# Optimization experiments

Measured on AMD Instinct MI355X. Metric: run time of the kernel, lower is better.

## Reference

```python
import jax, jax.numpy as jnp
import numpy as np

S, E, K, D = 50000, 20000, 128, 128  # students, exercises, knowledge, emb dim
NE = 800000                          # edges per polarity
B = 8192                             # batch of response logs
L = 3                                # gcn layers
TEMP, CONTROL = 0.2, 0.3


def setup_inputs() -> dict:
    key = jax.random.key(0)
    ks = jax.random.split(key, 40)

    def nrm(i, shape, scale=0.05):
        return jax.random.normal(ks[i], shape, jnp.float32) * scale

    def uni(i, shape):
        return jax.random.uniform(ks[i], shape, jnp.float32)

    inp = {
        'stu_id': jax.random.randint(ks[0], (B,), 0, S, jnp.int32),
        'exer_id': jax.random.randint(ks[1], (B,), 0, E, jnp.int32),
        'kn_emb': uni(2, (B, K)),
        'ui1_u': jax.random.randint(ks[3], (NE,), 0, S, jnp.int32),
        'ui1_i': jax.random.randint(ks[4], (NE,), 0, E, jnp.int32),
        'ui1_val': uni(5, (NE,)), 'iu1_val': uni(6, (NE,)),
        'eps_ui1': uni(7, (NE,)), 'eps_iu1': uni(8, (NE,)),
        'ui0_u': jax.random.randint(ks[9], (NE,), 0, S, jnp.int32),
        'ui0_i': jax.random.randint(ks[10], (NE,), 0, E, jnp.int32),
        'ui0_val': uni(11, (NE,)), 'iu0_val': uni(12, (NE,)),
        'eps_ui0': uni(13, (NE,)), 'eps_iu0': uni(14, (NE,)),
        # embeddings
        'student_emb': nrm(15, (S, D)), 'exercise_emb': nrm(16, (E, D)),
        'knowledge_emb': nrm(17, (K, D)),
        'stu_b': nrm(18, (S, 1)), 'exer_b': nrm(19, (E, 1)), 'disc': nrm(20, (E, 1)),
        # edge-gate MLPs (polarity 1 and 0)
        'W1_l1': nrm(21, (D, 2 * D)), 'b1_l1': jnp.zeros((D,), jnp.float32),
        'W2_l1': nrm(22, (1, D)), 'b2_l1': jnp.zeros((1,), jnp.float32),
        'W1_l0': nrm(23, (D, 2 * D)), 'b1_l0': jnp.zeros((D,), jnp.float32),
        'W2_l0': nrm(24, (1, D)), 'b2_l0': jnp.zeros((1,), jnp.float32),
        # PosLinear prednet
        'pw1': nrm(25, (256, K)), 'pb1': jnp.zeros((256,), jnp.float32),
        'pw2': nrm(26, (128, 256)), 'pb2': jnp.zeros((128,), jnp.float32),
        'pw3': nrm(27, (1, 128)), 'pb3': jnp.zeros((1,), jnp.float32),
    }
    return inp


def _gate(uids, iids, uemb, iemb, W1, b1, W2, b2, eps):
    # concrete-distribution edge gate; embeddings are detached in original code
    row = jax.lax.stop_gradient(uemb)[uids]          # [NE, D]
    col = jax.lax.stop_gradient(iemb)[iids]          # [NE, D]
    h = jax.nn.relu(jnp.concatenate([row, col], axis=1) @ W1.T + b1)
    logit = (h @ W2.T + b2).reshape(-1)              # [NE]
    eps = jnp.clip(eps, 1e-6, 1.0 - 1e-6)
    g = jnp.log(eps) - jnp.log1p(-eps)               # logistic noise
    return CONTROL * jax.nn.sigmoid((logit + g) / TEMP) + (1.0 - CONTROL)


def _spmm(rows, cols, vals, x, n_rows):
    # out[rows] += vals * x[cols]
    return jax.ops.segment_sum(vals[:, None] * x[cols], rows, num_segments=n_rows)


def _poslin(x, W, b):
    Wp = 2.0 * jax.nn.relu(-W) + W  # == |W|
    return x @ Wp.T + b


def reference(stu_id, exer_id, kn_emb, ui1_u, ui1_i, ui1_val, iu1_val, eps_ui1,
              eps_iu1, ui0_u, ui0_i, ui0_val, iu0_val, eps_ui0, eps_iu0,
              student_emb, exercise_emb, knowledge_emb, stu_b, exer_b, disc,
              W1_l1, b1_l1, W2_l1, b2_l1, W1_l0, b1_l0, W2_l0, b2_l0,
              pw1, pb1, pw2, pb2, pw3, pb3):
    # --- graph_learner: per-edge gates on all 4 sparse matrices ---
    v_ui1 = ui1_val * _gate(ui1_u, ui1_i, student_emb, exercise_emb, W1_l1, b1_l1, W2_l1, b2_l1, eps_ui1)
    v_iu1 = iu1_val * _gate(ui1_u, ui1_i, student_emb, exercise_emb, W1_l1, b1_l1, W2_l1, b2_l1, eps_iu1)
    v_ui0 = ui0_val * _gate(ui0_u, ui0_i, student_emb, exercise_emb, W1_l0, b1_l0, W2_l0, b2_l0, eps_ui0)
    v_iu0 = iu0_val * _gate(ui0_u, ui0_i, student_emb, exercise_emb, W1_l0, b1_l0, W2_l0, b2_l0, eps_iu0)

    # --- graph_representations: L rounds of sparse propagation, mean over layers ---
    stu, exer = student_emb, exercise_emb
    stu_sum, exer_sum = stu, exer
    for _ in range(L):
        u1 = _spmm(ui1_u, ui1_i, v_ui1, exer, S)
        i1 = _spmm(ui1_i, ui1_u, v_iu1, stu, E)
        u0 = _spmm(ui0_u, ui0_i, v_ui0, exer, S)
        i0 = _spmm(ui0_i, ui0_u, v_iu0, stu, E)
        stu, exer = u1 + u0, i1 + i0
        stu_sum = stu_sum + stu
        exer_sum = exer_sum + exer
    stu_final = stu_sum / (L + 1)
    exer_final = exer_sum / (L + 1)

    # --- NCDM-style prediction head with PosLinear MLP ---
    stat = jax.nn.sigmoid(stu_final[stu_id] @ knowledge_emb.T + stu_b[stu_id])   # [B, K]
    diff = jax.nn.sigmoid(exer_final[exer_id] @ knowledge_emb.T + exer_b[exer_id])
    e_d = jax.nn.sigmoid(disc[exer_id])                                          # [B, 1]
    x = e_d * (stat - diff) * kn_emb
    h = jax.nn.sigmoid(_poslin(x, pw1, pb1))
    h = jax.nn.sigmoid(_poslin(h, pw2, pb2))
    out = jax.nn.sigmoid(_poslin(h, pw3, pb3)).reshape(-1)                       # [B]
    return out
```

## Files before the change

### kernel.cpp

```cpp
#include <hip/hip_runtime.h>
#include <hip/hip_bf16.h>
#include <math.h>

#define S_N 50000
#define E_N 20000
#define K_N 128
#define D_N 128
#define NE_N 800000
#define B_N 8192
#define L_N 3
#define GATE_TILES (NE_N / 64)
#define NB_S 782
#define NB_E 313
#define BPAD 464
#define BSLACK 480

typedef __attribute__((ext_vector_type(4))) float floatx4;
typedef __attribute__((ext_vector_type(8))) short short8v;

__device__ __forceinline__ unsigned short f2bf(float x) {
  unsigned int u = __float_as_uint(x);
  u += 0x7FFFu + ((u >> 16) & 1u);
  return (unsigned short)(u >> 16);
}
__device__ __forceinline__ float bf2f(unsigned short u) {
  return __uint_as_float(((unsigned int)u) << 16);
}
__device__ __forceinline__ float sigm(float z) { return 1.0f / (1.0f + __expf(-z)); }

__device__ __forceinline__ unsigned char f2e4m3(float x) {
  unsigned int u = __float_as_uint(x);
  unsigned char s = (unsigned char)((u >> 24) & 0x80);
  int e = (int)((u >> 23) & 0xFF) - 127;
  unsigned int m = u & 0x7FFFFF;
  if (((u >> 23) & 0xFF) == 0) return s;
  if (e >= 9) return s | 0x7E;
  if (e < -10) return s;
  if (e >= -6) {
    unsigned int keep = m >> 20;
    unsigned int rest = m & 0xFFFFF;
    if (rest > 0x80000u || (rest == 0x80000u && (keep & 1))) keep++;
    if (keep == 8) { keep = 0; e++; if (e >= 9) return s | 0x7E; }
    unsigned char b = (unsigned char)(s | ((e + 7) << 3) | keep);
    if ((b & 0x7F) == 0x7F) b = s | 0x7E;
    return b;
  }
  int shift = -6 - e;
  unsigned int full = 0x800000u | m;
  unsigned int q = full >> (20 + shift);
  unsigned int rest = full & ((1u << (20 + shift)) - 1);
  unsigned int half = 1u << (19 + shift);
  if (rest > half || (rest == half && (q & 1))) q++;
  if (q == 8) return s | 0x08;
  return (unsigned char)(s | q);
}
__device__ __forceinline__ unsigned int pk4_fp8(float4 v) {
  return (unsigned int)f2e4m3(v.x) | ((unsigned int)f2e4m3(v.y) << 8) |
         ((unsigned int)f2e4m3(v.z) << 16) | ((unsigned int)f2e4m3(v.w) << 24);
}

__global__ void prep_kernel(const float* __restrict__ W1_l1, const float* __restrict__ W1_l0,
                            const float* __restrict__ pw1, const float* __restrict__ pw2,
                            const float* __restrict__ pw3, const float* __restrict__ ke,
                            unsigned int* __restrict__ w1f8_1, unsigned int* __restrict__ w1f8_0,
                            float* __restrict__ pw1T, float* __restrict__ pw2T,
                            float* __restrict__ pw3a, float* __restrict__ keT) {
  int i = blockIdx.x * blockDim.x + threadIdx.x;
  if (i < 8192) { w1f8_1[i] = pk4_fp8(((const float4*)W1_l1)[i]); return; }
  i -= 8192;
  if (i < 8192) { w1f8_0[i] = pk4_fp8(((const float4*)W1_l0)[i]); return; }
  i -= 8192;
  if (i < 32768) { int d = i >> 8, j = i & 255; pw1T[i] = fabsf(pw1[j * 128 + d]); return; }
  i -= 32768;
  if (i < 32768) { int d = i >> 7, j = i & 127; pw2T[i] = fabsf(pw2[j * 256 + d]); return; }
  i -= 32768;
  if (i < 128) { pw3a[i] = fabsf(pw3[i]); return; }
  i -= 128;
  if (i < 16384) { int d = i >> 7, k = i & 127; keT[i] = ke[k * 128 + d]; return; }
}

__global__ void init_bf_kernel(const float* __restrict__ se, const float* __restrict__ ee,
                               unsigned short* __restrict__ sbf, unsigned short* __restrict__ ebf,
                               unsigned int* __restrict__ sf8, unsigned int* __restrict__ ef8,
                               float* __restrict__ sS, float* __restrict__ eS) {
  int i = blockIdx.x * blockDim.x + threadIdx.x;
  const int nS4 = S_N * 32, nE4 = E_N * 32;
  if (i < nS4) {
    float4 v = ((const float4*)se)[i];
    ((float4*)sS)[i] = v;
    unsigned int lo = (unsigned int)f2bf(v.x) | ((unsigned int)f2bf(v.y) << 16);
    unsigned int hi = (unsigned int)f2bf(v.z) | ((unsigned int)f2bf(v.w) << 16);
    ((uint2*)sbf)[i] = make_uint2(lo, hi);
    sf8[i] = pk4_fp8(v);
    return;
  }
  i -= nS4;
  if (i < nE4) {
    float4 v = ((const float4*)ee)[i];
    ((float4*)eS)[i] = v;
    unsigned int lo = (unsigned int)f2bf(v.x) | ((unsigned int)f2bf(v.y) << 16);
    unsigned int hi = (unsigned int)f2bf(v.z) | ((unsigned int)f2bf(v.w) << 16);
    ((uint2*)ebf)[i] = make_uint2(lo, hi);
    ef8[i] = pk4_fp8(v);
  }
}

__global__ void zero_kernel(int* __restrict__ p, int n) {
  int i = blockIdx.x * blockDim.x + threadIdx.x;
  if (i < n) p[i] = 0;
}

__global__ __launch_bounds__(256)
void histB_kernel(const int* __restrict__ u1, const int* __restrict__ i1,
                  const int* __restrict__ u0, const int* __restrict__ i0,
                  int* __restrict__ gHistS, int* __restrict__ gHistE) {
  __shared__ int hS[NB_S], hE[NB_E];
  int t = threadIdx.x;
  for (int b = t; b < NB_S; b += 256) hS[b] = 0;
  for (int b = t; b < NB_E; b += 256) hE[b] = 0;
  __syncthreads();
  int e0 = blockIdx.x * 2048;
  for (int k = 0; k < 8; ++k) {
    int e = e0 + k * 256 + t;
    if (e < NE_N) {
      atomicAdd(&hS[u1[e] >> 6], 1);
      atomicAdd(&hS[u0[e] >> 6], 1);
      atomicAdd(&hE[i1[e] >> 6], 1);
      atomicAdd(&hE[i0[e] >> 6], 1);
    }
  }
  __syncthreads();
  for (int b = t; b < NB_S; b += 256) if (hS[b]) atomicAdd(&gHistS[b], hS[b]);
  for (int b = t; b < NB_E; b += 256) if (hE[b]) atomicAdd(&gHistE[b], hE[b]);
}

__global__ __launch_bounds__(128)
void scanB_kernel(const int* __restrict__ gHistS, int* __restrict__ baseS,
                  int* __restrict__ gCurS, int* __restrict__ basePS,
                  const int* __restrict__ gHistE, int* __restrict__ baseE,
                  int* __restrict__ gCurE, int* __restrict__ basePE) {
  int w = threadIdx.x >> 6, l = threadIdx.x & 63;
  int n = w ? NB_E : NB_S;
  const int* src = w ? gHistE : gHistS;
  int* bs  = w ? baseE  : baseS;
  int* cur = w ? gCurE  : gCurS;
  int* bsP = w ? basePE : basePS;
  int carry = 0, carryP = 0;
  for (int base = 0; base < n; base += 64) {
    int i = base + l;
    int v = (i < n) ? src[i] : 0;
    int p = (i < n) ? ((v + BPAD + 15) & ~15) : 0;
    int x = v, y = p;
#pragma unroll
    for (int o = 1; o < 64; o <<= 1) {
      int xx = __shfl_up(x, o, 64);
      int yy = __shfl_up(y, o, 64);
      if (l >= o) { x += xx; y += yy; }
    }
    if (i < n) {
      int ex = carry + x - v;
      bs[i] = ex; cur[i] = ex;
      bsP[i] = carryP + y - p;
    }
    carry += __shfl(x, 63, 64);
    carryP += __shfl(y, 63, 64);
  }
  if (l == 0) { bs[n] = carry; bsP[n] = carryP; }
}

__global__ __launch_bounds__(256)
void append_kernel(const int* __restrict__ u1, const int* __restrict__ i1,
                   const int* __restrict__ u0, const int* __restrict__ i0,
                   const float* __restrict__ v_ui1, const float* __restrict__ v_iu1,
                   const float* __restrict__ v_ui0, const float* __restrict__ v_iu0,
                   int* __restrict__ gCurS, int* __restrict__ gCurE,
                   int2* __restrict__ recS, int2* __restrict__ recE) {
  __shared__ int hS[NB_S], hE[NB_E];
  int t = threadIdx.x;
  for (int b = t; b < NB_S; b += 256) hS[b] = 0;
  for (int b = t; b < NB_E; b += 256) hE[b] = 0;
  __syncthreads();
  int e0 = blockIdx.x * 2048;
  for (int k = 0; k < 8; ++k) {
    int e = e0 + k * 256 + t;
    if (e < NE_N) {
      atomicAdd(&hS[u1[e] >> 6], 1);
      atomicAdd(&hS[u0[e] >> 6], 1);
      atomicAdd(&hE[i1[e] >> 6], 1);
      atomicAdd(&hE[i0[e] >> 6], 1);
    }
  }
  __syncthreads();
  for (int b = t; b < NB_S; b += 256) { int c = hS[b]; hS[b] = c ? atomicAdd(&gCurS[b], c) : 0; }
  for (int b = t; b < NB_E; b += 256) { int c = hE[b]; hE[b] = c ? atomicAdd(&gCurE[b], c) : 0; }
  __syncthreads();
  for (int k = 0; k < 8; ++k) {
    int e = e0 + k * 256 + t;
    if (e < NE_N) {
      int a = u1[e], b = i1[e], c = u0[e], d = i0[e];
      int s;
      s = atomicAdd(&hS[a >> 6], 1); recS[s] = make_int2(((a & 63) << 16) | b, __float_as_int(v_ui1[e]));
      s = atomicAdd(&hE[b >> 6], 1); recE[s] = make_int2(((b & 63) << 16) | a, __float_as_int(v_iu1[e]));
      s = atomicAdd(&hS[c >> 6], 1); recS[s] = make_int2(((c & 63) << 16) | d, __float_as_int(v_ui0[e]));
      s = atomicAdd(&hE[d >> 6], 1); recE[s] = make_int2(((d & 63) << 16) | c, __float_as_int(v_iu0[e]));
    }
  }
}

__global__ __launch_bounds__(256)
void sortRow_kernel(const int* __restrict__ baseIn, const int* __restrict__ basePad,
                    const int2* __restrict__ rin_all, int2* __restrict__ rout_all,
                    int* __restrict__ rowPtr, int* __restrict__ rowCnt8, int nRowsTot) {
  __shared__ int cntR[64], offR[64], curR[64];
  int b = blockIdx.x, t = threadIdx.x;
  int bi = baseIn[b], cnt = baseIn[b + 1] - bi;
  int bo = basePad[b];
  int row0 = b * 64;
  const int2* rin = rin_all + bi;
  int2* rout = rout_all + bo;
  if (t < 64) cntR[t] = 0;
  __syncthreads();
  for (int j = t; j < cnt; j += 256) atomicAdd(&cntR[(rin[j].x >> 16) & 63], 1);
  __syncthreads();
  if (t < 64) {
    int p = (cntR[t] + 7) & ~7;
    int x = p;
#pragma unroll
    for (int o = 1; o < 64; o <<= 1) { int y = __shfl_up(x, o, 64); if (t >= o) x += y; }
    int ex = x - p;
    offR[t] = ex; curR[t] = ex;
    if (row0 + t < nRowsTot) {
      rowPtr[row0 + t] = bo + ex;
      rowCnt8[row0 + t] = p >> 3;
    }
  }
  __syncthreads();
  for (int j = t; j < cnt; j += 256) {
    int2 rc = rin[j];
    int r = (rc.x >> 16) & 63;
    int slot = atomicAdd(&curR[r], 1);
    rout[slot] = make_int2(rc.x & 0xFFFF, rc.y);
  }
  __syncthreads();
  if (t < 64) {
    int c = cntR[t], p = (c + 7) & ~7, o = offR[t];
    for (int j = c; j < p; ++j) rout[o + j] = make_int2(0, 0);
  }
}

__global__ __launch_bounds__(512, 2)
void gate_kernel(const int* __restrict__ eu1, const int* __restrict__ ei1,
                 const int* __restrict__ eu0, const int* __restrict__ ei0,
                 const unsigned char* __restrict__ sf8, const unsigned char* __restrict__ ef8,
                 const unsigned char* __restrict__ w1f8_1, const unsigned char* __restrict__ w1f8_0,
                 const float* __restrict__ b1_1, const float* __restrict__ w2_1,
                 const float* __restrict__ b2_1,
                 const float* __restrict__ b1_0, const float* __restrict__ w2_0,
                 const float* __restrict__ b2_0,
                 float* __restrict__ logit1, float* __restrict__ logit0) {
  __shared__ unsigned char Xl[64 * 272];
  __shared__ float plds[8][16];
  const int* eu; const int* ei; const unsigned char* w1f8;
  const float *b1p, *w2p, *b2p; float* lg;
  if (blockIdx.x < 2048) {
    eu = eu1; ei = ei1; w1f8 = w1f8_1; b1p = b1_1; w2p = w2_1; b2p = b2_1; lg = logit1;
  } else {
    eu = eu0; ei = ei0; w1f8 = w1f8_0; b1p = b1_0; w2p = w2_0; b2p = b2_0; lg = logit0;
  }
  int bb = blockIdx.x & 2047;
  int t = threadIdx.x;
  int wv = t >> 6, l = t & 63;
  int sub = l & 15, grp = l >> 4;
  int nh = wv & 1, rg = wv >> 1;

  long bfrag[4][8];
#pragma unroll
  for (int nt = 0; nt < 4; ++nt) {
    int col = nh * 64 + nt * 16 + sub;
#pragma unroll
    for (int ks = 0; ks < 8; ++ks)
      bfrag[nt][ks] = *(const long*)&w1f8[(col << 8) + ks * 32 + grp * 8];
  }
  float b1v[4], w2v[4];
#pragma unroll
  for (int nt = 0; nt < 4; ++nt) {
    int col = nh * 64 + nt * 16 + sub;
    b1v[nt] = b1p[col];
    w2v[nt] = w2p[col];
  }
  float b2s = b2p[0];

  for (int tile = bb; tile < GATE_TILES; tile += 2048) {
    int e0 = tile * 64;
    {
      int el = t >> 3, q = t & 7;
      int eIdx = e0 + el;
      const unsigned char* srcrow = (q < 4)
          ? sf8 + (size_t)eu[eIdx] * 128 + q * 32
          : ef8 + (size_t)ei[eIdx] * 128 + (q - 4) * 32;
      uint4 c0 = ((const uint4*)srcrow)[0];
      uint4 c1 = ((const uint4*)srcrow)[1];
      *(uint4*)&Xl[el * 272 + q * 32] = c0;
      *(uint4*)&Xl[el * 272 + q * 32 + 16] = c1;
    }
    __syncthreads();

    floatx4 zero4 = {0.f, 0.f, 0.f, 0.f};
    floatx4 acc[4] = {zero4, zero4, zero4, zero4};
#pragma unroll
    for (int ks = 0; ks < 8; ++ks) {
      long a = *(const long*)&Xl[(rg * 16 + sub) * 272 + ks * 32 + grp * 8];
#pragma unroll
      for (int nt = 0; nt < 4; ++nt)
        acc[nt] = __builtin_amdgcn_mfma_f32_16x16x32_fp8_fp8(a, bfrag[nt][ks], acc[nt], 0, 0, 0);
    }
    float p0 = 0, p1 = 0, p2 = 0, p3 = 0;
#pragma unroll
    for (int nt = 0; nt < 4; ++nt) {
      float bb2 = b1v[nt], ww = w2v[nt];
      p0 += fmaxf(acc[nt][0] + bb2, 0.0f) * ww;
      p1 += fmaxf(acc[nt][1] + bb2, 0.0f) * ww;
      p2 += fmaxf(acc[nt][2] + bb2, 0.0f) * ww;
      p3 += fmaxf(acc[nt][3] + bb2, 0.0f) * ww;
    }
#pragma unroll
    for (int m = 1; m < 16; m <<= 1) {
      p0 += __shfl_xor(p0, m, 64);
      p1 += __shfl_xor(p1, m, 64);
      p2 += __shfl_xor(p2, m, 64);
      p3 += __shfl_xor(p3, m, 64);
    }
    if (sub < 4) {
      float pv = (sub == 0) ? p0 : (sub == 1) ? p1 : (sub == 2) ? p2 : p3;
      plds[wv][grp * 4 + sub] = pv;
    }
    __syncthreads();
    if (wv == 0)
      lg[e0 + l] = plds[(l >> 4) * 2][l & 15] + plds[(l >> 4) * 2 + 1][l & 15] + b2s;
    __syncthreads();
  }
}

__global__ __launch_bounds__(256)
void gatefin_kernel(const float* __restrict__ logit1, const float* __restrict__ logit0,
                    const float* __restrict__ ui1_val, const float* __restrict__ iu1_val,
                    const float* __restrict__ eps_ui1, const float* __restrict__ eps_iu1,
                    const float* __restrict__ ui0_val, const float* __restrict__ iu0_val,
                    const float* __restrict__ eps_ui0, const float* __restrict__ eps_iu0,
                    float* __restrict__ v_ui1, float* __restrict__ v_iu1,
                    float* __restrict__ v_ui0, float* __restrict__ v_iu0) {
  int e = blockIdx.x * 256 + threadIdx.x;
  if (e >= NE_N) return;
  float lg1 = logit1[e], lg0 = logit0[e];
  float ep, g, s;
  ep = fminf(fmaxf(eps_ui1[e], 1e-6f), 1.0f - 1e-6f);
  g = __logf(ep) - log1pf(-ep);
  s = 1.0f / (1.0f + __expf(-(lg1 + g) * 5.0f));
  v_ui1[e] = ui1_val[e] * (0.3f * s + 0.7f);
  ep = fminf(fmaxf(eps_iu1[e], 1e-6f), 1.0f - 1e-6f);
  g = __logf(ep) - log1pf(-ep);
  s = 1.0f / (1.0f + __expf(-(lg1 + g) * 5.0f));
  v_iu1[e] = iu1_val[e] * (0.3f * s + 0.7f);
  ep = fminf(fmaxf(eps_ui0[e], 1e-6f), 1.0f - 1e-6f);
  g = __logf(ep) - log1pf(-ep);
  s = 1.0f / (1.0f + __expf(-(lg0 + g) * 5.0f));
  v_ui0[e] = ui0_val[e] * (0.3f * s + 0.7f);
  ep = fminf(fmaxf(eps_iu0[e], 1e-6f), 1.0f - 1e-6f);
  g = __logf(ep) - log1pf(-ep);
  s = 1.0f / (1.0f + __expf(-(lg0 + g) * 5.0f));
  v_iu0[e] = iu0_val[e] * (0.3f * s + 0.7f);
}

__global__ __launch_bounds__(256)
void spmm_csr_kernel(const int* __restrict__ rowPtrS, const int* __restrict__ rowCnt8S,
                     const int2* __restrict__ rec2S,
                     const int* __restrict__ rowPtrE, const int* __restrict__ rowCnt8E,
                     const int2* __restrict__ rec2E,
                     const unsigned short* __restrict__ scur, const unsigned short* __restrict__ ecur,
                     unsigned short* __restrict__ snxt, unsigned short* __restrict__ enxt,
                     float* __restrict__ stuS, float* __restrict__ exeS) {
  int gw = (blockIdx.x * 256 + threadIdx.x) >> 6;
  int l = threadIdx.x & 63;
  int g = l >> 3, lane8 = l & 7;
  if (gw >= S_N + E_N) return;
  const int2* rec; const unsigned short* src; unsigned short* dst; float* sum;
  const int* rp; const int* rc8; int r;
  if (gw < S_N) { r = gw;       rp = rowPtrS; rc8 = rowCnt8S; rec = rec2S; src = ecur; dst = snxt; sum = stuS; }
  else          { r = gw - S_N; rp = rowPtrE; rc8 = rowCnt8E; rec = rec2E; src = scur; dst = enxt; sum = exeS; }
  int s0 = rp[r], n8 = rc8[r];
  float acc[16];
#pragma unroll
  for (int i = 0; i < 16; ++i) acc[i] = 0.f;
  for (int k = 0; k < n8; ++k) {
    int2 e = rec[s0 + k * 8 + g];
    float val = __int_as_float(e.y);
    const uint4* rowp = (const uint4*)(src + (size_t)e.x * 128);
    uint4 q0 = rowp[lane8 * 2];
    uint4 q1 = rowp[lane8 * 2 + 1];
#pragma unroll
    for (int i = 0; i < 4; ++i) {
      unsigned int w = ((const unsigned int*)&q0)[i];
      acc[2 * i]     = fmaf(val, bf2f((unsigned short)(w & 0xFFFF)), acc[2 * i]);
      acc[2 * i + 1] = fmaf(val, bf2f((unsigned short)(w >> 16)),    acc[2 * i + 1]);
    }
#pragma unroll
    for (int i = 0; i < 4; ++i) {
      unsigned int w = ((const unsigned int*)&q1)[i];
      acc[8 + 2 * i]     = fmaf(val, bf2f((unsigned short)(w & 0xFFFF)), acc[8 + 2 * i]);
      acc[8 + 2 * i + 1] = fmaf(val, bf2f((unsigned short)(w >> 16)),    acc[8 + 2 * i + 1]);
    }
  }
#pragma unroll
  for (int m = 8; m < 64; m <<= 1) {
#pragma unroll
    for (int i = 0; i < 16; ++i) acc[i] += __shfl_xor(acc[i], m, 64);
  }
  if (g == 0) {
    size_t base = (size_t)r * 128 + lane8 * 16;
    short8v o0, o1;
#pragma unroll
    for (int i = 0; i < 8; ++i) { o0[i] = (short)f2bf(acc[i]); o1[i] = (short)f2bf(acc[8 + i]); }
    *(short8v*)(dst + base) = o0;
    *(short8v*)(dst + base + 8) = o1;
    float4* sp = (float4*)(sum + base);
#pragma unroll
    for (int i = 0; i < 4; ++i) {
      float4 s = sp[i];
      s.x += acc[4 * i]; s.y += acc[4 * i + 1]; s.z += acc[4 * i + 2]; s.w += acc[4 * i + 3];
      sp[i] = s;
    }
  }
}

__global__ __launch_bounds__(256)
void head1_kernel(const int* __restrict__ stu_id, const int* __restrict__ exer_id,
                  const float* __restrict__ kn, const float* __restrict__ stuS,
                  const float* __restrict__ exeS, const float* __restrict__ keT,
                  const float* __restrict__ stub, const float* __restrict__ exeb,
                  const float* __restrict__ disc, float* __restrict__ xbuf) {
  __shared__ float srw[4][128], erw[4][128];
  int wv = threadIdx.x >> 6, l = threadIdx.x & 63;
  int b = blockIdx.x * 4 + wv;
  int sid = stu_id[b], eid = exer_id[b];
  float2 sv = ((const float2*)(stuS + (size_t)sid * 128))[l];
  float2 ev = ((const float2*)(exeS + (size_t)eid * 128))[l];
  srw[wv][2 * l] = sv.x * 0.25f; srw[wv][2 * l + 1] = sv.y * 0.25f;
  erw[wv][2 * l] = ev.x * 0.25f; erw[wv][2 * l + 1] = ev.y * 0.25f;
  __syncthreads();
  float s0 = 0, s1 = 0, d0 = 0, d1 = 0;
  for (int d = 0; d < 128; ++d) {
    float sd = srw[wv][d], ed = erw[wv][d];
    float ka = keT[d * 128 + l], kb = keT[d * 128 + l + 64];
    s0 = fmaf(sd, ka, s0); s1 = fmaf(sd, kb, s1);
    d0 = fmaf(ed, ka, d0); d1 = fmaf(ed, kb, d1);
  }
  float sbv = stub[sid], ebv = exeb[eid];
  float edv = sigm(disc[eid]);
  float st0 = sigm(s0 + sbv), st1 = sigm(s1 + sbv);
  float df0 = sigm(d0 + ebv), df1 = sigm(d1 + ebv);
  xbuf[(size_t)b * 128 + l]      = edv * (st0 - df0) * kn[(size_t)b * 128 + l];
  xbuf[(size_t)b * 128 + l + 64] = edv * (st1 - df1) * kn[(size_t)b * 128 + l + 64];
}

__global__ __launch_bounds__(256)
void head2_kernel(const float* __restrict__ xbuf, const float* __restrict__ pw1T,
                  const float* __restrict__ pb1, const float* __restrict__ pw2T,
                  const float* __restrict__ pb2, const float* __restrict__ pw3a,
                  const float* __restrict__ pb3, float* __restrict__ out) {
  __shared__ float xs[4][128], h1s[4][256], h2s[4][128];
  int wv = threadIdx.x >> 6, l = threadIdx.x & 63;
  int b = blockIdx.x * 4 + wv;
  xs[wv][l] = xbuf[(size_t)b * 128 + l];
  xs[wv][l + 64] = xbuf[(size_t)b * 128 + l + 64];
  __syncthreads();
#pragma unroll
  for (int q = 0; q < 4; ++q) {
    int j = q * 64 + l;
    float acc = 0.f;
    for (int d = 0; d < 128; ++d) acc = fmaf(xs[wv][d], pw1T[d * 256 + j], acc);
    h1s[wv][j] = sigm(acc + pb1[j]);
  }
  __syncthreads();
#pragma unroll
  for (int q = 0; q < 2; ++q) {
    int j = q * 64 + l;
    float acc = 0.f;
    for (int d = 0; d < 256; ++d) acc = fmaf(h1s[wv][d], pw2T[d * 128 + j], acc);
    h2s[wv][j] = sigm(acc + pb2[j]);
  }
  __syncthreads();
  float p = h2s[wv][l] * pw3a[l] + h2s[wv][l + 64] * pw3a[l + 64];
#pragma unroll
  for (int m = 1; m < 64; m <<= 1) p += __shfl_xor(p, m, 64);
  if (l == 0) out[b] = sigm(p + pb3[0]);
}

extern "C" void kernel_launch(void* const* d_in, const int* in_sizes, int n_in,
                              void* d_out, int out_size, void* d_ws, size_t ws_size,
                              hipStream_t stream) {
  const int*   stu_id  = (const int*)  d_in[0];
  const int*   exer_id = (const int*)  d_in[1];
  const float* kn_emb  = (const float*)d_in[2];
  const int*   ui1_u   = (const int*)  d_in[3];
  const int*   ui1_i   = (const int*)  d_in[4];
  const float* ui1_val = (const float*)d_in[5];
  const float* iu1_val = (const float*)d_in[6];
  const float* eps_ui1 = (const float*)d_in[7];
  const float* eps_iu1 = (const float*)d_in[8];
  const int*   ui0_u   = (const int*)  d_in[9];
  const int*   ui0_i   = (const int*)  d_in[10];
  const float* ui0_val = (const float*)d_in[11];
  const float* iu0_val = (const float*)d_in[12];
  const float* eps_ui0 = (const float*)d_in[13];
  const float* eps_iu0 = (const float*)d_in[14];
  const float* stu_emb = (const float*)d_in[15];
  const float* exe_emb = (const float*)d_in[16];
  const float* kno_emb = (const float*)d_in[17];
  const float* stu_b   = (const float*)d_in[18];
  const float* exe_b   = (const float*)d_in[19];
  const float* disc    = (const float*)d_in[20];
  const float* W1_l1   = (const float*)d_in[21];
  const float* b1_l1   = (const float*)d_in[22];
  const float* W2_l1   = (const float*)d_in[23];
  const float* b2_l1   = (const float*)d_in[24];
  const float* W1_l0   = (const float*)d_in[25];
  const float* b1_l0   = (const float*)d_in[26];
  const float* W2_l0   = (const float*)d_in[27];
  const float* b2_l0   = (const float*)d_in[28];
  const float* pw1     = (const float*)d_in[29];
  const float* pb1     = (const float*)d_in[30];
  const float* pw2     = (const float*)d_in[31];
  const float* pb2     = (const float*)d_in[32];
  const float* pw3     = (const float*)d_in[33];
  const float* pb3     = (const float*)d_in[34];
  float* out = (float*)d_out;
  (void)in_sizes; (void)n_in; (void)out_size; (void)ws_size;

  size_t off = 0;
  char* base = (char*)d_ws;
  auto carve = [&](size_t bytes) -> char* {
    char* p = base + off;
    off += (bytes + 255) & ~(size_t)255;
    return p;
  };
  unsigned int* w1f8_1 = (unsigned int*)carve(8192 * 4);
  unsigned int* w1f8_0 = (unsigned int*)carve(8192 * 4);
  float* pw1T = (float*)carve(32768 * 4);
  float* pw2T = (float*)carve(32768 * 4);
  float* pw3a = (float*)carve(128 * 4);
  float* keT  = (float*)carve(16384 * 4);
  float* v_ui1 = (float*)carve((size_t)2 * NE_N * 8 + (size_t)BSLACK * NB_S * 8);
  float* v_iu1 = v_ui1 + NE_N;
  float* v_ui0 = v_iu1 + NE_N;
  float* v_iu0 = v_ui0 + NE_N;
  unsigned short* stuBfA = (unsigned short*)carve((size_t)S_N * 128 * 2);
  unsigned short* stuBfB = (unsigned short*)carve((size_t)S_N * 128 * 2);
  unsigned short* exeBfA = (unsigned short*)carve((size_t)E_N * 128 * 2);
  unsigned short* exeBfB = (unsigned short*)carve((size_t)E_N * 128 * 2);
  unsigned int* sf8 = (unsigned int*)carve((size_t)S_N * 32 * 4);
  unsigned int* ef8 = (unsigned int*)carve((size_t)E_N * 32 * 4);
  float* stuS = (float*)carve((size_t)S_N * 128 * 4);
  float* exeS = (float*)carve((size_t)E_N * 128 * 4);
  float* logit1 = (float*)carve((size_t)NE_N * 4);
  float* logit0 = (float*)carve((size_t)NE_N * 4);
  int* gHistS = (int*)carve((size_t)(NB_S + NB_E) * 4);
  int* gHistE = gHistS + NB_S;
  int* baseSb  = (int*)carve((size_t)(NB_S + 1) * 4);
  int* baseEb  = (int*)carve((size_t)(NB_E + 1) * 4);
  int* basePSb = (int*)carve((size_t)(NB_S + 1) * 4);
  int* basePEb = (int*)carve((size_t)(NB_E + 1) * 4);
  int* gCurS  = (int*)carve((size_t)NB_S * 4);
  int* gCurE  = (int*)carve((size_t)NB_E * 4);
  int2* recS = (int2*)carve((size_t)2 * NE_N * 8 + (size_t)BSLACK * NB_E * 8);
  int2* recE = (int2*)carve((size_t)2 * NE_N * 8);
  int* rowPtrS  = (int*)carve((size_t)S_N * 4);
  int* rowCnt8S = (int*)carve((size_t)S_N * 4);
  int* rowPtrE  = (int*)carve((size_t)E_N * 4);
  int* rowCnt8E = (int*)carve((size_t)E_N * 4);
  float* xbuf = (float*)carve((size_t)B_N * 128 * 4);
  int2* rec2S = (int2*)v_ui1;
  int2* rec2E = recS;

  prep_kernel<<<(98432 + 255) / 256, 256, 0, stream>>>(W1_l1, W1_l0, pw1, pw2, pw3, kno_emb,
                                                       w1f8_1, w1f8_0, pw1T, pw2T, pw3a, keT);
  init_bf_kernel<<<(2240000 + 255) / 256, 256, 0, stream>>>(stu_emb, exe_emb, stuBfA, exeBfA,
                                                            sf8, ef8, stuS, exeS);
  zero_kernel<<<(NB_S + NB_E + 255) / 256, 256, 0, stream>>>(gHistS, NB_S + NB_E);
  histB_kernel<<<(NE_N + 2047) / 2048, 256, 0, stream>>>(ui1_u, ui1_i, ui0_u, ui0_i,
                                                         gHistS, gHistE);
  scanB_kernel<<<1, 128, 0, stream>>>(gHistS, baseSb, gCurS, basePSb,
                                      gHistE, baseEb, gCurE, basePEb);
  gate_kernel<<<4096, 512, 0, stream>>>(ui1_u, ui1_i, ui0_u, ui0_i,
                                        (const unsigned char*)sf8, (const unsigned char*)ef8,
                                        (const unsigned char*)w1f8_1, (const unsigned char*)w1f8_0,
                                        b1_l1, W2_l1, b2_l1, b1_l0, W2_l0, b2_l0,
                                        logit1, logit0);
  gatefin_kernel<<<(NE_N + 255) / 256, 256, 0, stream>>>(logit1, logit0,
                                                         ui1_val, iu1_val, eps_ui1, eps_iu1,
                                                         ui0_val, iu0_val, eps_ui0, eps_iu0,
                                                         v_ui1, v_iu1, v_ui0, v_iu0);
  append_kernel<<<(NE_N + 2047) / 2048, 256, 0, stream>>>(ui1_u, ui1_i, ui0_u, ui0_i,
                                                          v_ui1, v_iu1, v_ui0, v_iu0,
                                                          gCurS, gCurE, recS, recE);
  sortRow_kernel<<<NB_S, 256, 0, stream>>>(baseSb, basePSb, recS, rec2S,
                                           rowPtrS, rowCnt8S, S_N);
  sortRow_kernel<<<NB_E, 256, 0, stream>>>(baseEb, basePEb, recE, rec2E,
                                           rowPtrE, rowCnt8E, E_N);
  const unsigned short* scur = stuBfA; const unsigned short* ecur = exeBfA;
  unsigned short* snxt = stuBfB; unsigned short* enxt = exeBfB;
  for (int layer = 0; layer < L_N; ++layer) {
    spmm_csr_kernel<<<(S_N + E_N + 3) / 4, 256, 0, stream>>>(
        rowPtrS, rowCnt8S, rec2S, rowPtrE, rowCnt8E, rec2E,
        scur, ecur, snxt, enxt, stuS, exeS);
    const unsigned short* t1 = scur; scur = snxt; snxt = (unsigned short*)t1;
    const unsigned short* t2 = ecur; ecur = enxt; enxt = (unsigned short*)t2;
  }
  head1_kernel<<<B_N / 4, 256, 0, stream>>>(stu_id, exer_id, kn_emb, stuS, exeS, keT,
                                            stu_b, exe_b, disc, xbuf);
  head2_kernel<<<B_N / 4, 256, 0, stream>>>(xbuf, pw1T, pb1, pw2T, pb2, pw3a, pb3, out);
}
```

Before: 704.8 us.

## Fuse gate finalization into append kernel and double-buffer gate tile gathers

The separate gatefin kernel is removed. Its concrete-distribution sigmoid and value scaling now run inside append_kernel, which reads the logits, eps and val arrays directly, so the four intermediate v_* arrays are no longer written to and re-read from global memory. The gate kernel also gets a double-buffered LDS tile: the next tile's gathered embedding rows are loaded into registers while MFMAs run on the current tile, which drops one barrier per iteration. This costs twice the LDS per block and extra live registers, which may reduce occupancy.

```diff
diff --git a/kernel.cpp b/kernel.cpp
--- a/kernel.cpp
+++ b/kernel.cpp
@@ -168,11 +168,122 @@
   if (l == 0) { bs[n] = carry; bsP[n] = carryP; }
 }
 
+__global__ __launch_bounds__(512, 2)
+void gate_kernel(const int* __restrict__ eu1, const int* __restrict__ ei1,
+                 const int* __restrict__ eu0, const int* __restrict__ ei0,
+                 const unsigned char* __restrict__ sf8, const unsigned char* __restrict__ ef8,
+                 const unsigned char* __restrict__ w1f8_1, const unsigned char* __restrict__ w1f8_0,
+                 const float* __restrict__ b1_1, const float* __restrict__ w2_1,
+                 const float* __restrict__ b2_1,
+                 const float* __restrict__ b1_0, const float* __restrict__ w2_0,
+                 const float* __restrict__ b2_0,
+                 float* __restrict__ logit1, float* __restrict__ logit0) {
+  __shared__ unsigned char Xl[2][64 * 272];
+  __shared__ float plds[8][16];
+  const int* eu; const int* ei; const unsigned char* w1f8;
+  const float *b1p, *w2p, *b2p; float* lg;
+  if (blockIdx.x < 2048) {
+    eu = eu1; ei = ei1; w1f8 = w1f8_1; b1p = b1_1; w2p = w2_1; b2p = b2_1; lg = logit1;
+  } else {
+    eu = eu0; ei = ei0; w1f8 = w1f8_0; b1p = b1_0; w2p = w2_0; b2p = b2_0; lg = logit0;
+  }
+  int bb = blockIdx.x & 2047;
+  int t = threadIdx.x;
+  int wv = t >> 6, l = t & 63;
+  int sub = l & 15, grp = l >> 4;
+  int nh = wv & 1, rg = wv >> 1;
+  int el = t >> 3, q = t & 7;
+
+  long bfrag[4][8];
+#pragma unroll
+  for (int nt = 0; nt < 4; ++nt) {
+    int col = nh * 64 + nt * 16 + sub;
+#pragma unroll
+    for (int ks = 0; ks < 8; ++ks)
+      bfrag[nt][ks] = *(const long*)&w1f8[(col << 8) + ks * 32 + grp * 8];
+  }
+  float b1v[4], w2v[4];
+#pragma unroll
+  for (int nt = 0; nt < 4; ++nt) {
+    int col = nh * 64 + nt * 16 + sub;
+    b1v[nt] = b1p[col];
+    w2v[nt] = w2p[col];
+  }
+  float b2s = b2p[0];
+
+  uint4 c0, c1;
+  {
+    int eIdx = bb * 64 + el;
+    const unsigned char* srcrow = (q < 4)
+        ? sf8 + (size_t)eu[eIdx] * 128 + q * 32
+        : ef8 + (size_t)ei[eIdx] * 128 + (q - 4) * 32;
+    c0 = ((const uint4*)srcrow)[0];
+    c1 = ((const uint4*)srcrow)[1];
+    *(uint4*)&Xl[0][el * 272 + q * 32] = c0;
+    *(uint4*)&Xl[0][el * 272 + q * 32 + 16] = c1;
+  }
+  int parity = 0;
+  for (int tile = bb; tile < GATE_TILES; tile += 2048) {
+    int nxt = tile + 2048;
+    bool hasNext = (nxt < GATE_TILES);
+    if (hasNext) {
+      int eIdx = nxt * 64 + el;
+      const unsigned char* srcrow = (q < 4)
+          ? sf8 + (size_t)eu[eIdx] * 128 + q * 32
+          : ef8 + (size_t)ei[eIdx] * 128 + (q - 4) * 32;
+      c0 = ((const uint4*)srcrow)[0];
+      c1 = ((const uint4*)srcrow)[1];
+    }
+    __syncthreads();
+
+    floatx4 zero4 = {0.f, 0.f, 0.f, 0.f};
+    floatx4 acc[4] = {zero4, zero4, zero4, zero4};
+#pragma unroll
+    for (int ks = 0; ks < 8; ++ks) {
+      long a = *(const long*)&Xl[parity][(rg * 16 + sub) * 272 + ks * 32 + grp * 8];
+#pragma unroll
+      for (int nt = 0; nt < 4; ++nt)
+        acc[nt] = __builtin_amdgcn_mfma_f32_16x16x32_fp8_fp8(a, bfrag[nt][ks], acc[nt], 0, 0, 0);
+    }
+    float p0 = 0, p1 = 0, p2 = 0, p3 = 0;
+#pragma unroll
+    for (int nt = 0; nt < 4; ++nt) {
+      float bb2 = b1v[nt], ww = w2v[nt];
+      p0 += fmaxf(acc[nt][0] + bb2, 0.0f) * ww;
+      p1 += fmaxf(acc[nt][1] + bb2, 0.0f) * ww;
+      p2 += fmaxf(acc[nt][2] + bb2, 0.0f) * ww;
+      p3 += fmaxf(acc[nt][3] + bb2, 0.0f) * ww;
+    }
+#pragma unroll
+    for (int m = 1; m < 16; m <<= 1) {
+      p0 += __shfl_xor(p0, m, 64);
+      p1 += __shfl_xor(p1, m, 64);
+      p2 += __shfl_xor(p2, m, 64);
+      p3 += __shfl_xor(p3, m, 64);
+    }
+    if (sub < 4) {
+      float pv = (sub == 0) ? p0 : (sub == 1) ? p1 : (sub == 2) ? p2 : p3;
+      plds[wv][grp * 4 + sub] = pv;
+    }
+    __syncthreads();
+    if (wv == 0)
+      lg[tile * 64 + l] = plds[(l >> 4) * 2][l & 15] + plds[(l >> 4) * 2 + 1][l & 15] + b2s;
+    if (hasNext) {
+      *(uint4*)&Xl[parity ^ 1][el * 272 + q * 32] = c0;
+      *(uint4*)&Xl[parity ^ 1][el * 272 + q * 32 + 16] = c1;
+    }
+    parity ^= 1;
+  }
+}
+
 __global__ __launch_bounds__(256)
 void append_kernel(const int* __restrict__ u1, const int* __restrict__ i1,
                    const int* __restrict__ u0, const int* __restrict__ i0,
-                   const float* __restrict__ v_ui1, const float* __restrict__ v_iu1,
-                   const float* __restrict__ v_ui0, const float* __restrict__ v_iu0,
+                   const float* __restrict__ logit1, const float* __restrict__ logit0,
+                   const float* __restrict__ ui1_val, const float* __restrict__ iu1_val,
+                   const float* __restrict__ eps_ui1, const float* __restrict__ eps_iu1,
+                   const float* __restrict__ ui0_val, const float* __restrict__ iu0_val,
+                   const float* __restrict__ eps_ui0, const float* __restrict__ eps_iu0,
                    int* __restrict__ gCurS, int* __restrict__ gCurE,
                    int2* __restrict__ recS, int2* __restrict__ recE) {
   __shared__ int hS[NB_S], hE[NB_E];
@@ -198,11 +309,29 @@
     int e = e0 + k * 256 + t;
     if (e < NE_N) {
       int a = u1[e], b = i1[e], c = u0[e], d = i0[e];
+      float lg1 = logit1[e], lg0 = logit0[e];
+      float ep, g, s2;
+      ep = fminf(fmaxf(eps_ui1[e], 1e-6f), 1.0f - 1e-6f);
+      g = __logf(ep) - log1pf(-ep);
+      s2 = 1.0f / (1.0f + __expf(-(lg1 + g) * 5.0f));
+      float v_ui1 = ui1_val[e] * (0.3f * s2 + 0.7f);
+      ep = fminf(fmaxf(eps_iu1[e], 1e-6f), 1.0f - 1e-6f);
+      g = __logf(ep) - log1pf(-ep);
+      s2 = 1.0f / (1.0f + __expf(-(lg1 + g) * 5.0f));
+      float v_iu1 = iu1_val[e] * (0.3f * s2 + 0.7f);
+      ep = fminf(fmaxf(eps_ui0[e], 1e-6f), 1.0f - 1e-6f);
+      g = __logf(ep) - log1pf(-ep);
+      s2 = 1.0f / (1.0f + __expf(-(lg0 + g) * 5.0f));
+      float v_ui0 = ui0_val[e] * (0.3f * s2 + 0.7f);
+      ep = fminf(fmaxf(eps_iu0[e], 1e-6f), 1.0f - 1e-6f);
+      g = __logf(ep) - log1pf(-ep);
+      s2 = 1.0f / (1.0f + __expf(-(lg0 + g) * 5.0f));
+      float v_iu0 = iu0_val[e] * (0.3f * s2 + 0.7f);
       int s;
-      s = atomicAdd(&hS[a >> 6], 1); recS[s] = make_int2(((a & 63) << 16) | b, __float_as_int(v_ui1[e]));
-      s = atomicAdd(&hE[b >> 6], 1); recE[s] = make_int2(((b & 63) << 16) | a, __float_as_int(v_iu1[e]));
-      s = atomicAdd(&hS[c >> 6], 1); recS[s] = make_int2(((c & 63) << 16) | d, __float_as_int(v_ui0[e]));
-      s = atomicAdd(&hE[d >> 6], 1); recE[s] = make_int2(((d & 63) << 16) | c, __float_as_int(v_iu0[e]));
+      s = atomicAdd(&hS[a >> 6], 1); recS[s] = make_int2(((a & 63) << 16) | b, __float_as_int(v_ui1));
+      s = atomicAdd(&hE[b >> 6], 1); recE[s] = make_int2(((b & 63) << 16) | a, __float_as_int(v_iu1));
+      s = atomicAdd(&hS[c >> 6], 1); recS[s] = make_int2(((c & 63) << 16) | d, __float_as_int(v_ui0));
+      s = atomicAdd(&hE[d >> 6], 1); recE[s] = make_int2(((d & 63) << 16) | c, __float_as_int(v_iu0));
     }
   }
 }
@@ -246,129 +375,6 @@
     int c = cntR[t], p = (c + 7) & ~7, o = offR[t];
     for (int j = c; j < p; ++j) rout[o + j] = make_int2(0, 0);
   }
-}
-
-__global__ __launch_bounds__(512, 2)
-void gate_kernel(const int* __restrict__ eu1, const int* __restrict__ ei1,
-                 const int* __restrict__ eu0, const int* __restrict__ ei0,
-                 const unsigned char* __restrict__ sf8, const unsigned char* __restrict__ ef8,
-                 const unsigned char* __restrict__ w1f8_1, const unsigned char* __restrict__ w1f8_0,
-                 const float* __restrict__ b1_1, const float* __restrict__ w2_1,
-                 const float* __restrict__ b2_1,
-                 const float* __restrict__ b1_0, const float* __restrict__ w2_0,
-                 const float* __restrict__ b2_0,
-                 float* __restrict__ logit1, float* __restrict__ logit0) {
-  __shared__ unsigned char Xl[64 * 272];
-  __shared__ float plds[8][16];
-  const int* eu; const int* ei; const unsigned char* w1f8;
-  const float *b1p, *w2p, *b2p; float* lg;
-  if (blockIdx.x < 2048) {
-    eu = eu1; ei = ei1; w1f8 = w1f8_1; b1p = b1_1; w2p = w2_1; b2p = b2_1; lg = logit1;
-  } else {
-    eu = eu0; ei = ei0; w1f8 = w1f8_0; b1p = b1_0; w2p = w2_0; b2p = b2_0; lg = logit0;
-  }
-  int bb = blockIdx.x & 2047;
-  int t = threadIdx.x;
-  int wv = t >> 6, l = t & 63;
-  int sub = l & 15, grp = l >> 4;
-  int nh = wv & 1, rg = wv >> 1;
-
-  long bfrag[4][8];
-#pragma unroll
-  for (int nt = 0; nt < 4; ++nt) {
-    int col = nh * 64 + nt * 16 + sub;
-#pragma unroll
-    for (int ks = 0; ks < 8; ++ks)
-      bfrag[nt][ks] = *(const long*)&w1f8[(col << 8) + ks * 32 + grp * 8];
-  }
-  float b1v[4], w2v[4];
-#pragma unroll
-  for (int nt = 0; nt < 4; ++nt) {
-    int col = nh * 64 + nt * 16 + sub;
-    b1v[nt] = b1p[col];
-    w2v[nt] = w2p[col];
-  }
-  float b2s = b2p[0];
-
-  for (int tile = bb; tile < GATE_TILES; tile += 2048) {
-    int e0 = tile * 64;
-    {
-      int el = t >> 3, q = t & 7;
-      int eIdx = e0 + el;
-      const unsigned char* srcrow = (q < 4)
-          ? sf8 + (size_t)eu[eIdx] * 128 + q * 32
-          : ef8 + (size_t)ei[eIdx] * 128 + (q - 4) * 32;
-      uint4 c0 = ((const uint4*)srcrow)[0];
-      uint4 c1 = ((const uint4*)srcrow)[1];
-      *(uint4*)&Xl[el * 272 + q * 32] = c0;
-      *(uint4*)&Xl[el * 272 + q * 32 + 16] = c1;
-    }
-    __syncthreads();
-
-    floatx4 zero4 = {0.f, 0.f, 0.f, 0.f};
-    floatx4 acc[4] = {zero4, zero4, zero4, zero4};
-#pragma unroll
-    for (int ks = 0; ks < 8; ++ks) {
-      long a = *(const long*)&Xl[(rg * 16 + sub) * 272 + ks * 32 + grp * 8];
-#pragma unroll
-      for (int nt = 0; nt < 4; ++nt)
-        acc[nt] = __builtin_amdgcn_mfma_f32_16x16x32_fp8_fp8(a, bfrag[nt][ks], acc[nt], 0, 0, 0);
-    }
-    float p0 = 0, p1 = 0, p2 = 0, p3 = 0;
-#pragma unroll
-    for (int nt = 0; nt < 4; ++nt) {
-      float bb2 = b1v[nt], ww = w2v[nt];
-      p0 += fmaxf(acc[nt][0] + bb2, 0.0f) * ww;
-      p1 += fmaxf(acc[nt][1] + bb2, 0.0f) * ww;
-      p2 += fmaxf(acc[nt][2] + bb2, 0.0f) * ww;
-      p3 += fmaxf(acc[nt][3] + bb2, 0.0f) * ww;
-    }
-#pragma unroll
-    for (int m = 1; m < 16; m <<= 1) {
-      p0 += __shfl_xor(p0, m, 64);
-      p1 += __shfl_xor(p1, m, 64);
-      p2 += __shfl_xor(p2, m, 64);
-      p3 += __shfl_xor(p3, m, 64);
-    }
-    if (sub < 4) {
-      float pv = (sub == 0) ? p0 : (sub == 1) ? p1 : (sub == 2) ? p2 : p3;
-      plds[wv][grp * 4 + sub] = pv;
-    }
-    __syncthreads();
-    if (wv == 0)
-      lg[e0 + l] = plds[(l >> 4) * 2][l & 15] + plds[(l >> 4) * 2 + 1][l & 15] + b2s;
-    __syncthreads();
-  }
-}
-
-__global__ __launch_bounds__(256)
-void gatefin_kernel(const float* __restrict__ logit1, const float* __restrict__ logit0,
-                    const float* __restrict__ ui1_val, const float* __restrict__ iu1_val,
-                    const float* __restrict__ eps_ui1, const float* __restrict__ eps_iu1,
-                    const float* __restrict__ ui0_val, const float* __restrict__ iu0_val,
-                    const float* __restrict__ eps_ui0, const float* __restrict__ eps_iu0,
-                    float* __restrict__ v_ui1, float* __restrict__ v_iu1,
-                    float* __restrict__ v_ui0, float* __restrict__ v_iu0) {
-  int e = blockIdx.x * 256 + threadIdx.x;
-  if (e >= NE_N) return;
-  float lg1 = logit1[e], lg0 = logit0[e];
-  float ep, g, s;
-  ep = fminf(fmaxf(eps_ui1[e], 1e-6f), 1.0f - 1e-6f);
-  g = __logf(ep) - log1pf(-ep);
-  s = 1.0f / (1.0f + __expf(-(lg1 + g) * 5.0f));
-  v_ui1[e] = ui1_val[e] * (0.3f * s + 0.7f);
-  ep = fminf(fmaxf(eps_iu1[e], 1e-6f), 1.0f - 1e-6f);
-  g = __logf(ep) - log1pf(-ep);
-  s = 1.0f / (1.0f + __expf(-(lg1 + g) * 5.0f));
-  v_iu1[e] = iu1_val[e] * (0.3f * s + 0.7f);
-  ep = fminf(fmaxf(eps_ui0[e], 1e-6f), 1.0f - 1e-6f);
-  g = __logf(ep) - log1pf(-ep);
-  s = 1.0f / (1.0f + __expf(-(lg0 + g) * 5.0f));
-  v_ui0[e] = ui0_val[e] * (0.3f * s + 0.7f);
-  ep = fminf(fmaxf(eps_iu0[e], 1e-6f), 1.0f - 1e-6f);
-  g = __logf(ep) - log1pf(-ep);
-  s = 1.0f / (1.0f + __expf(-(lg0 + g) * 5.0f));
-  v_iu0[e] = iu0_val[e] * (0.3f * s + 0.7f);
 }
 
 __global__ __launch_bounds__(256)
@@ -549,10 +555,7 @@
   float* pw2T = (float*)carve(32768 * 4);
   float* pw3a = (float*)carve(128 * 4);
   float* keT  = (float*)carve(16384 * 4);
-  float* v_ui1 = (float*)carve((size_t)2 * NE_N * 8 + (size_t)BSLACK * NB_S * 8);
-  float* v_iu1 = v_ui1 + NE_N;
-  float* v_ui0 = v_iu1 + NE_N;
-  float* v_iu0 = v_ui0 + NE_N;
+  char* vblock = carve((size_t)2 * NE_N * 8 + (size_t)BSLACK * NB_S * 8);
   unsigned short* stuBfA = (unsigned short*)carve((size_t)S_N * 128 * 2);
   unsigned short* stuBfB = (unsigned short*)carve((size_t)S_N * 128 * 2);
   unsigned short* exeBfA = (unsigned short*)carve((size_t)E_N * 128 * 2);
@@ -578,7 +581,7 @@
   int* rowPtrE  = (int*)carve((size_t)E_N * 4);
   int* rowCnt8E = (int*)carve((size_t)E_N * 4);
   float* xbuf = (float*)carve((size_t)B_N * 128 * 4);
-  int2* rec2S = (int2*)v_ui1;
+  int2* rec2S = (int2*)vblock;
   int2* rec2E = recS;
 
   prep_kernel<<<(98432 + 255) / 256, 256, 0, stream>>>(W1_l1, W1_l0, pw1, pw2, pw3, kno_emb,
@@ -595,12 +598,10 @@
                                         (const unsigned char*)w1f8_1, (const unsigned char*)w1f8_0,
                                         b1_l1, W2_l1, b2_l1, b1_l0, W2_l0, b2_l0,
                                         logit1, logit0);
-  gatefin_kernel<<<(NE_N + 255) / 256, 256, 0, stream>>>(logit1, logit0,
-                                                         ui1_val, iu1_val, eps_ui1, eps_iu1,
-                                                         ui0_val, iu0_val, eps_ui0, eps_iu0,
-                                                         v_ui1, v_iu1, v_ui0, v_iu0);
   append_kernel<<<(NE_N + 2047) / 2048, 256, 0, stream>>>(ui1_u, ui1_i, ui0_u, ui0_i,
-                                                          v_ui1, v_iu1, v_ui0, v_iu0,
+                                                          logit1, logit0,
+                                                          ui1_val, iu1_val, eps_ui1, eps_iu1,
+                                                          ui0_val, iu0_val, eps_ui0, eps_iu0,
                                                           gCurS, gCurE, recS, recE);
   sortRow_kernel<<<NB_S, 256, 0, stream>>>(baseSb, basePSb, recS, rec2S,
                                            rowPtrS, rowCnt8S, S_N);
```

New measurement: 692.9 us. No clear change (-1.7%).
